# Kernel tuning notes

Hardware: AMD Instinct MI355X
Metric: run time of the kernel (lower is better)

The kernel has to match this reference:

```python
import jax, jax.numpy as jnp
import numpy as np

N_HEADS = 2
EPS = 1e-5
NEG_SLOPE = 0.02
N_CENTROIDS = 1024
RADII = (0.1, 0.2)
KS = (32, 64)


def fps(x, m):
    # Farthest point sampling (deterministic start at index 0). x: [B, C, N]
    B, C, N = x.shape
    def body(carry, _):
        distance, farthest = carry
        centroid = jnp.take_along_axis(x, jnp.broadcast_to(farthest[:, None, None], (B, C, 1)), axis=2)
        dist = jnp.sum((x - centroid) ** 2, axis=1)  # [B, N]
        distance = jnp.minimum(distance, dist)
        nxt = jnp.argmax(distance, axis=1).astype(jnp.int32)
        return (distance, nxt), farthest
    init = (jnp.full((B, N), 1e10, x.dtype), jnp.zeros((B,), jnp.int32))
    _, idxs = jax.lax.scan(body, init, None, length=m)
    return idxs.T  # [B, m]


def ball_group(x, centroids, radius, k):
    # x: [B, C, N], centroids: [B, C, M] -> (idx [B,M,k] int32, mask [B,M,k] bool)
    B, C, N = x.shape
    M = centroids.shape[2]
    d = (jnp.sum(x * x, axis=1)[:, None, :]
         - 2.0 * jnp.einsum('bcm,bcn->bmn', centroids, x)
         + jnp.sum(centroids * centroids, axis=1)[:, :, None])  # [B, M, N]
    idx = jnp.broadcast_to(jnp.arange(N, dtype=jnp.int32)[None, None, :], (B, M, N))
    idx = jnp.where(d > radius * radius, N, idx)
    idx = -jax.lax.top_k(-idx, k)[0]  # k smallest indices, ascending (matches torch.topk largest=False)
    mask = idx == N
    first = jnp.where(idx[:, :, :1] == N, 0, idx[:, :, :1])
    idx = jnp.where(mask, jnp.broadcast_to(first, idx.shape), idx)
    return idx, mask


def attention_mix(x, y, mask, wq, wk, wv, wo):
    # x: [B, C, K] centroids, y: [B, C, K, Np] groups, mask: [B, K, Np]
    B, C, K = x.shape
    Np = y.shape[3]
    H = N_HEADS
    q = jnp.einsum('oc,bck->bok', wq, x).reshape(B, H, C, K)
    kk = jnp.einsum('oc,bckn->bokn', wk, y).reshape(B, H, C, K, Np)
    v = jnp.einsum('oc,bckn->bokn', wv, y).reshape(B, H, C, K, Np)
    w = jnp.einsum('bhck,bhckn->bhkn', q, kk) / (C ** 0.5)
    w = jnp.where(mask[:, None, :, :], -1e9, w)
    w = jax.nn.softmax(w, axis=3)
    o = jnp.einsum('bhkn,bhckn->bhck', w, v).reshape(B, H * C, K)
    return jnp.einsum('oc,bck->bok', wo, o) + x


def conv_bn(x, w, b, g, beta, act):
    # 1x1 Conv1d + BatchNorm1d (training-mode batch stats) + optional LeakyReLU(0.02)
    x = jnp.einsum('oc,bck->bok', w, x) + b[None, :, None]
    mu = jnp.mean(x, axis=(0, 2), keepdims=True)
    var = jnp.var(x, axis=(0, 2), keepdims=True)
    x = (x - mu) * jax.lax.rsqrt(var + EPS) * g[None, :, None] + beta[None, :, None]
    return jnp.where(x > 0, x, NEG_SLOPE * x) if act else x


def pointnet_msg(xyz, point_features, attn_params, mlp_params):
    support = jnp.concatenate([xyz, point_features], axis=1)  # [B, 32, N]
    B, Cs, N = support.shape
    M = N_CENTROIDS
    cidx = fps(support, M)  # [B, M]
    centroids = jnp.take_along_axis(support, jnp.broadcast_to(cidx[:, None, :], (B, Cs, M)), axis=2)
    new_xyz = jnp.take_along_axis(xyz, jnp.broadcast_to(cidx[:, None, :], (B, 3, M)), axis=2)
    feats = []
    for s, (radius, k) in enumerate(zip(RADII, KS)):
        idx, mask = ball_group(support, centroids, radius, k)  # [B, M, k]
        gidx = jnp.broadcast_to(idx.reshape(B, 1, M * k), (B, Cs, M * k))
        group = jnp.take_along_axis(support, gidx, axis=2).reshape(B, Cs, M, k)
        group = group - centroids[:, :, :, None]
        f = attention_mix(centroids, group, mask, *attn_params[s])
        (w0, b0, g0, t0), (w1, b1, g1, t1) = mlp_params[s]
        f = conv_bn(f, w0, b0, g0, t0, act=True)
        f = conv_bn(f, w1, b1, g1, t1, act=False)
        feats.append(f)
    return new_xyz, jnp.concatenate(feats, axis=1)  # [B,3,M], [B,256,M]


def setup_inputs() -> dict:
    key = jax.random.key(0)
    ks = jax.random.split(key, 32)
    B, N, C = 4, 16384, 32
    d = {}
    d['xyz'] = jax.random.uniform(ks[0], (B, 3, N), jnp.float32)
    d['point_features'] = jax.random.normal(ks[1], (B, C - 3, N), jnp.float32)
    i = 2
    for s in range(2):
        d[f'aq{s}'] = 0.05 * jax.random.normal(ks[i], (64, 32), jnp.float32); i += 1
        d[f'ak{s}'] = 0.05 * jax.random.normal(ks[i], (64, 32), jnp.float32); i += 1
        d[f'av{s}'] = 0.05 * jax.random.normal(ks[i], (64, 32), jnp.float32); i += 1
        d[f'ao{s}'] = 0.05 * jax.random.normal(ks[i], (32, 64), jnp.float32); i += 1
        d[f'mw{s}0'] = 0.05 * jax.random.normal(ks[i], (64, 32), jnp.float32); i += 1
        d[f'mb{s}0'] = jnp.zeros((64,), jnp.float32)
        d[f'mg{s}0'] = jnp.ones((64,), jnp.float32)
        d[f'mbt{s}0'] = jnp.zeros((64,), jnp.float32)
        d[f'mw{s}1'] = 0.05 * jax.random.normal(ks[i], (128, 64), jnp.float32); i += 1
        d[f'mb{s}1'] = jnp.zeros((128,), jnp.float32)
        d[f'mg{s}1'] = jnp.ones((128,), jnp.float32)
        d[f'mbt{s}1'] = jnp.zeros((128,), jnp.float32)
    return d


def reference(xyz, point_features,
              aq0, ak0, av0, ao0, mw00, mb00, mg00, mbt00, mw01, mb01, mg01, mbt01,
              aq1, ak1, av1, ao1, mw10, mb10, mg10, mbt10, mw11, mb11, mg11, mbt11):
    attn_params = (((aq0, ak0, av0, ao0)), ((aq1, ak1, av1, ao1)))
    mlp_params = (((mw00, mb00, mg00, mbt00), (mw01, mb01, mg01, mbt01)),
                  ((mw10, mb10, mg10, mbt10), (mw11, mb11, mg11, mbt11)))
    return pointnet_msg(xyz, point_features, attn_params, mlp_params)
```

## Files before the change

kernel.cpp:

```cpp
#include <hip/hip_runtime.h>
#include <hip/hip_bf16.h>


static constexpr int Bb = 4;
static constexpr int Npts = 16384;
static constexpr int Mc = 1024;
static constexpr int NBLK = 16;
static constexpr int OUT_EXPECT = 12288 + 1048576;
#define BN_EPS 1e-5f
#define SLOPE 0.02f
#define SCOPE_AGT __HIP_MEMORY_SCOPE_AGENT

static constexpr size_t OFF_STATS = 33024;
static constexpr size_t OFF_GCNT  = 40960;
static constexpr size_t ZERO_BYTES = 65536;
static constexpr size_t OFF_CIDX  = 65536;
static constexpr size_t OFF_IDX0  = 81920;
static constexpr size_t OFF_CNT0  = 344064;
static constexpr size_t OFF_IDX1  = 360448;
static constexpr size_t OFF_CNT1  = 884736;
static constexpr size_t OFF_ATTN  = 901120;
static constexpr size_t OFF_Z0    = 1163264;
static constexpr size_t WS_REQUIRED = 1687552;
static constexpr size_t OFF_FSLOT = 901120;
static constexpr size_t FSLOT_BYTES = (size_t)Bb * Mc * NBLK * 8;
static constexpr size_t OFF_Z1 = 1687552;
static constexpr size_t OFF_GENT = OFF_Z1;
static constexpr size_t WS_Z1_REQUIRED = OFF_Z1 + (size_t)Bb * 128 * Mc * 4;
static constexpr size_t OFF_SUPT = WS_Z1_REQUIRED;
static constexpr size_t WS_T_REQUIRED = OFF_SUPT + (size_t)Bb * Npts * 32 * 4;

__device__ __forceinline__ float sup_at(const float* xyz, const float* pf,
                                        int b, int c, int n) {
  return (c < 3) ? xyz[((size_t)b*3 + c)*Npts + n]
                 : pf[((size_t)b*29 + (c-3))*Npts + n];
}

__device__ __forceinline__ float sanf(float v, float repl) {
  if (!(v == v) || fabsf(v) > 1e30f) v = repl;
  return v;
}

__global__ __launch_bounds__(256) void fill_kernel(float* out, int n, float val) {
  int i = blockIdx.x * 256 + threadIdx.x;
  if (i < n) out[i] = val;
}

__global__ __launch_bounds__(256) void buildT_kernel(
    const float* __restrict__ xyz, const float* __restrict__ pf,
    float* __restrict__ supT) {
  int idx = blockIdx.x * 256 + threadIdx.x;
  int n = idx & (Npts - 1);
  int b = idx >> 14;
  float* dst = supT + ((size_t)b * Npts + n) * 32;
#pragma unroll
  for (int c = 0; c < 32; ++c) dst[c] = sup_at(xyz, pf, b, c, n);
}

__global__ __launch_bounds__(512, 2) void fps_ball_kernel(
    const float* __restrict__ xyz, const float* __restrict__ pf,
    const float* __restrict__ supT,
    unsigned int* __restrict__ cidx, unsigned long long* __restrict__ slots,
    unsigned int* __restrict__ gcnt, unsigned int* __restrict__ gent) {
  const int tid = threadIdx.x;
  if (blockIdx.x < 64) {
    const int blk = blockIdx.x;
    const int b = blk >> 4;
    const int sb = blk & (NBLK - 1);
    const int lane = tid & 63, wid = tid >> 6;
    float f0[32], f1[32];
    const int p0 = sb * 1024 + tid;
    const int p1 = p0 + 512;
    float d0 = 1e10f, d1 = 1e10f;
#pragma unroll
    for (int c = 0; c < 32; ++c) {
      f0[c] = sup_at(xyz, pf, b, c, p0);
      f1[c] = sup_at(xyz, pf, b, c, p1);
    }
    __shared__ float cf[32];
    __shared__ unsigned long long red[8];
    if (sb == 0 && tid == 0) atomicExch(&cidx[b * Mc], 0u);
    if (tid < 32) cf[tid] = sup_at(xyz, pf, b, tid, 0);
    __syncthreads();
    unsigned long long* slotb = slots + (size_t)b * Mc * NBLK;
    const float* supTb = supT + (size_t)b * Npts * 32;
    for (int it = 0; it < Mc - 1; ++it) {
      float cc[32];
#pragma unroll
      for (int c = 0; c < 32; ++c) cc[c] = cf[c];
      {
        float d = 0.f, e = 0.f;
#pragma unroll
        for (int c = 0; c < 32; ++c) {
          float t0 = f0[c] - cc[c];
          float s0 = __fmul_rn(t0, t0);
          d = (c == 0) ? s0 : __fadd_rn(d, s0);
          float t1 = f1[c] - cc[c];
          float s1 = __fmul_rn(t1, t1);
          e = (c == 0) ? s1 : __fadd_rn(e, s1);
        }
        d0 = fminf(d0, d);
        d1 = fminf(d1, e);
      }
      float bd; int bp;
      if (d0 >= d1) { bd = d0; bp = p0; } else { bd = d1; bp = p1; }
      unsigned long long v =
          ((unsigned long long)__float_as_uint(bd) << 32) | (unsigned int)(~(unsigned int)bp);
#pragma unroll
      for (int d = 32; d; d >>= 1) {
        unsigned long long o = __shfl_xor(v, d, 64);
        if (o > v) v = o;
      }
      if (lane == 0) red[wid] = v;
      __syncthreads();
      if (tid == 0) {
        unsigned long long vb = red[0];
#pragma unroll
        for (int w = 1; w < 8; ++w) if (red[w] > vb) vb = red[w];
        atomicMax(&slotb[(size_t)it * NBLK + sb], vb);
      }
      if (wid == 0) {
        unsigned long long myv = 0;
        if (lane < NBLK) {
          const unsigned long long* sp = &slotb[(size_t)it * NBLK + lane];
          while ((myv = __hip_atomic_load(sp, __ATOMIC_RELAXED, SCOPE_AGT)) == 0ull)
            __builtin_amdgcn_s_sleep(1);
        }
        unsigned long long mv = myv;
#pragma unroll
        for (int d = 8; d; d >>= 1) {
          unsigned long long o = __shfl_xor(mv, d, 16);
          if (o > mv) mv = o;
        }
        unsigned long long vwin = __shfl(mv, 0, 64);
        int idxWin = (int)(~(unsigned int)(vwin & 0xffffffffu)) & (Npts - 1);
        if (lane < 32) cf[lane] = supTb[(size_t)idxWin * 32 + lane];
        if (lane == 0 && sb == 0)
          atomicExch(&cidx[b * Mc + it + 1], (unsigned int)idxWin);
      }
      __syncthreads();
    }
  } else {
    const int blk2 = blockIdx.x - 64;
    const int b = blk2 >> 5;
    const int chunk = blk2 & 31;
    const int p = chunk * 512 + tid;
    const float* supTb = supT + (size_t)b * Npts * 32;
    float x[32];
    const float* srow = supTb + (size_t)p * 32;
#pragma unroll
    for (int c = 0; c < 32; ++c) x[c] = srow[c];
    float sp = 0.f;
#pragma unroll
    for (int c = 0; c < 32; ++c) sp = fmaf(x[c], x[c], sp);
    __shared__ float cfb[2][32];
    unsigned int* cidxb = cidx + b * Mc;
    unsigned int* gcntb = gcnt + b * Mc;
    unsigned int* gentb = gent + (size_t)b * Mc * 128;
    for (int m = 0; m < Mc; ++m) {
      if (tid < 32) {
        unsigned int ci;
        const unsigned int* cp = &cidxb[m];
        while ((ci = __hip_atomic_load(cp, __ATOMIC_RELAXED, SCOPE_AGT)) == 0xFFFFFFFFu)
          __builtin_amdgcn_s_sleep(2);
        cfb[m & 1][tid] = supTb[(size_t)(ci & (Npts - 1)) * 32 + tid];
      }
      __syncthreads();
      const float* cfm = cfb[m & 1];
      float csq = 0.f, dot = 0.f;
#pragma unroll
      for (int c = 0; c < 32; ++c) {
        csq = fmaf(cfm[c], cfm[c], csq);
        dot = fmaf(cfm[c], x[c], dot);
      }
      float d = sp - 2.0f * dot + csq;
      if (d <= 0.04f) {
        int pos = atomicAdd(&gcntb[m], 1u);
        if (pos < 128)
          gentb[(size_t)m * 128 + pos] = (unsigned int)p | (d <= 0.01f ? 0x80000000u : 0u);
      }
    }
  }
}

__global__ __launch_bounds__(256) void ballpost_kernel(
    unsigned int* __restrict__ gcnt, unsigned int* __restrict__ gent,
    unsigned short* __restrict__ idx0, int* __restrict__ cnt0,
    unsigned short* __restrict__ idx1, int* __restrict__ cnt1) {
  int idx = blockIdx.x * 256 + threadIdx.x;
  int b = idx >> 10;
  int m = idx & (Mc - 1);
  int gm = b * Mc + m;
  unsigned int* e = gent + (size_t)gm * 128;
  int nn = (int)gcnt[gm]; if (nn > 128) nn = 128;
  for (int i = 1; i < nn; ++i) {
    unsigned int ei = e[i]; unsigned int key = ei & 0x7fffffffu;
    int j = i - 1;
    while (j >= 0 && (e[j] & 0x7fffffffu) > key) { e[j+1] = e[j]; --j; }
    e[j+1] = ei;
  }
  int c1 = nn < 64 ? nn : 64;
  unsigned short first1 = nn > 0 ? (unsigned short)(e[0] & 0x7fffffffu) : 0;
  unsigned short* o1 = idx1 + (size_t)gm * 64;
  for (int j = 0; j < 64; ++j)
    o1[j] = j < c1 ? (unsigned short)(e[j] & 0x7fffffffu) : first1;
  cnt1[gm] = c1;
  unsigned short* o0 = idx0 + (size_t)gm * 32;
  int c0 = 0; unsigned short first0 = 0;
  for (int i = 0; i < nn && c0 < 32; ++i) {
    if (e[i] & 0x80000000u) {
      unsigned short nv = (unsigned short)(e[i] & 0x7fffffffu);
      if (c0 == 0) first0 = nv;
      o0[c0++] = nv;
    }
  }
  for (int j = c0; j < 32; ++j) o0[j] = first0;
  cnt0[gm] = c0;
}

__global__ __launch_bounds__(512, 2) void fps_kernel(
    const float* __restrict__ xyz, const float* __restrict__ pf,
    const float* __restrict__ supT,
    int* __restrict__ cidx, unsigned long long* __restrict__ slots) {
  const int blk = blockIdx.x;
  const int b = blk >> 4;
  const int sb = blk & (NBLK - 1);
  const int tid = threadIdx.x;
  const int lane = tid & 63, wid = tid >> 6;
  float f0[32], f1[32];
  const int p0 = sb * 1024 + tid;
  const int p1 = p0 + 512;
  float d0 = 1e10f, d1 = 1e10f;
#pragma unroll
  for (int c = 0; c < 32; ++c) {
    f0[c] = sup_at(xyz, pf, b, c, p0);
    f1[c] = sup_at(xyz, pf, b, c, p1);
  }
  __shared__ float cf[32];
  __shared__ unsigned long long red[8];
  if (sb == 0 && tid == 0) cidx[b * Mc] = 0;
  if (tid < 32) cf[tid] = sup_at(xyz, pf, b, tid, 0);
  __syncthreads();
  unsigned long long* slotb = slots + (size_t)b * Mc * NBLK;
  const float* supTb = supT ? supT + (size_t)b * Npts * 32 : nullptr;
  for (int it = 0; it < Mc - 1; ++it) {
    float cc[32];
#pragma unroll
    for (int c = 0; c < 32; ++c) cc[c] = cf[c];
    {
      float d = 0.f, e = 0.f;
#pragma unroll
      for (int c = 0; c < 32; ++c) {
        float t0 = f0[c] - cc[c];
        float s0 = __fmul_rn(t0, t0);
        d = (c == 0) ? s0 : __fadd_rn(d, s0);
        float t1 = f1[c] - cc[c];
        float s1 = __fmul_rn(t1, t1);
        e = (c == 0) ? s1 : __fadd_rn(e, s1);
      }
      d0 = fminf(d0, d);
      d1 = fminf(d1, e);
    }
    float bd; int bp;
    if (d0 >= d1) { bd = d0; bp = p0; } else { bd = d1; bp = p1; }
    unsigned long long v =
        ((unsigned long long)__float_as_uint(bd) << 32) | (unsigned int)(~(unsigned int)bp);
#pragma unroll
    for (int d = 32; d; d >>= 1) {
      unsigned long long o = __shfl_xor(v, d, 64);
      if (o > v) v = o;
    }
    if (lane == 0) red[wid] = v;
    __syncthreads();
    if (tid == 0) {
      unsigned long long vb = red[0];
#pragma unroll
      for (int w = 1; w < 8; ++w) if (red[w] > vb) vb = red[w];
      atomicMax(&slotb[(size_t)it * NBLK + sb], vb);
    }
    if (wid == 0) {
      unsigned long long myv = 0;
      if (lane < NBLK) {
        const unsigned long long* sp = &slotb[(size_t)it * NBLK + lane];
        while ((myv = __hip_atomic_load(sp, __ATOMIC_RELAXED, SCOPE_AGT)) == 0ull)
          __builtin_amdgcn_s_sleep(1);
      }
      unsigned long long mv = myv;
#pragma unroll
      for (int d = 8; d; d >>= 1) {
        unsigned long long o = __shfl_xor(mv, d, 16);
        if (o > mv) mv = o;
      }
      unsigned long long vwin = __shfl(mv, 0, 64);
      int idxWin = (int)(~(unsigned int)(vwin & 0xffffffffu)) & (Npts - 1);
      if (lane < 32)
        cf[lane] = supTb ? supTb[(size_t)idxWin * 32 + lane]
                         : sup_at(xyz, pf, b, lane, idxWin);
      if (lane == 0 && sb == 0) cidx[b * Mc + it + 1] = idxWin;
    }
    __syncthreads();
  }
}

__global__ __launch_bounds__(256) void gather_kernel(
    const float* __restrict__ xyz, const int* __restrict__ cidx,
    float* __restrict__ oxyz, int out_size) {
  int idx = blockIdx.x * 256 + threadIdx.x;
  if (idx >= out_size || idx >= 12288) return;
  int m = idx & (Mc - 1);
  int t = idx >> 10;
  int b = t / 3;
  int ci = cidx[b * Mc + m] & (Npts - 1);
  oxyz[idx] = sanf(xyz[(size_t)t * Npts + ci], 888.0f);
}

__global__ __launch_bounds__(256) void ball_kernel(
    const float* __restrict__ xyz, const float* __restrict__ pf,
    const int* __restrict__ cidx,
    unsigned short* __restrict__ idx0, int* __restrict__ cnt0,
    unsigned short* __restrict__ idx1, int* __restrict__ cnt1) {
  const int b = blockIdx.x >> 6;
  const int mt = blockIdx.x & 63;
  const int tid = threadIdx.x;
  __shared__ float cf[16][32];
  __shared__ float csq[16];
  __shared__ unsigned int ent[16][128];
  __shared__ int lcnt[16];
  for (int i = tid; i < 16 * 32; i += 256) {
    int ml = i >> 5, c = i & 31;
    int ci = cidx[b * Mc + mt * 16 + ml] & (Npts - 1);
    cf[ml][c] = sup_at(xyz, pf, b, c, ci);
  }
  if (tid < 16) lcnt[tid] = 0;
  __syncthreads();
  if (tid < 16) {
    float a = 0.f;
#pragma unroll
    for (int c = 0; c < 32; ++c) a = fmaf(cf[tid][c], cf[tid][c], a);
    csq[tid] = a;
  }
  __syncthreads();
  for (int ch = 0; ch < Npts / 256; ++ch) {
    int p = ch * 256 + tid;
    float x[32];
#pragma unroll
    for (int c = 0; c < 32; ++c) x[c] = sup_at(xyz, pf, b, c, p);
    float sp = 0.f;
#pragma unroll
    for (int c = 0; c < 32; ++c) sp = fmaf(x[c], x[c], sp);
#pragma unroll 4
    for (int ml = 0; ml < 16; ++ml) {
      float dot = 0.f;
#pragma unroll
      for (int c = 0; c < 32; ++c) dot = fmaf(cf[ml][c], x[c], dot);
      float d = sp - 2.0f * dot + csq[ml];
      if (d <= 0.04f) {
        int pos = atomicAdd(&lcnt[ml], 1);
        if (pos < 128) ent[ml][pos] = (unsigned int)p | (d <= 0.01f ? 0x80000000u : 0u);
      }
    }
  }
  __syncthreads();
  if (tid < 16) {
    int ml = tid;
    int nn = lcnt[ml]; if (nn > 128) nn = 128;
    for (int i = 1; i < nn; ++i) {
      unsigned int e = ent[ml][i]; unsigned int key = e & 0x7fffffffu;
      int j = i - 1;
      while (j >= 0 && (ent[ml][j] & 0x7fffffffu) > key) { ent[ml][j+1] = ent[ml][j]; --j; }
      ent[ml][j+1] = e;
    }
    int gm = b * Mc + mt * 16 + ml;
    int c1 = nn < 64 ? nn : 64;
    unsigned short first1 = nn > 0 ? (unsigned short)(ent[ml][0] & 0x7fffffffu) : 0;
    unsigned short* o1 = idx1 + (size_t)gm * 64;
    for (int j = 0; j < 64; ++j)
      o1[j] = j < c1 ? (unsigned short)(ent[ml][j] & 0x7fffffffu) : first1;
    cnt1[gm] = c1;
    unsigned short* o0 = idx0 + (size_t)gm * 32;
    int c0 = 0; unsigned short first0 = 0;
    for (int i = 0; i < nn && c0 < 32; ++i) {
      if (ent[ml][i] & 0x80000000u) {
        unsigned short nv = (unsigned short)(ent[ml][i] & 0x7fffffffu);
        if (c0 == 0) first0 = nv;
        o0[c0++] = nv;
      }
    }
    for (int j = c0; j < 32; ++j) o0[j] = first0;
    cnt0[gm] = c0;
  }
}

template <int K>
__global__ __launch_bounds__(256) void attn_kernel(
    const float* __restrict__ xyz, const float* __restrict__ pf,
    const float* __restrict__ supT,
    const int* __restrict__ cidx,
    const unsigned short* __restrict__ idxS, const int* __restrict__ cntS,
    const float* __restrict__ wq, const float* __restrict__ wk,
    const float* __restrict__ wv, const float* __restrict__ wo,
    __hip_bfloat16* __restrict__ outA) {
  __shared__ float WqL[64*33], WkL[64*33], WvL[64*33], WoL[32*65];
  __shared__ float xv[4][32];
  __shared__ float qv[4][64];
  __shared__ float yb[4][2][32];
  __shared__ float ov[4][64];
  __shared__ int cns[4];
  const int tid = threadIdx.x;
  const int wid = tid >> 6, lane = tid & 63;
  const int gid = blockIdx.x;
  const int b = gid >> 8;
  const int m = ((gid & 255) << 2) + wid;
  const float* supTb = supT ? supT + (size_t)b * Npts * 32 : nullptr;
  for (int i = tid; i < 2048; i += 256) {
    int r = i >> 5, c = i & 31;
    WqL[r*33 + c] = wq[i];
    WkL[r*33 + c] = wk[i];
    WvL[r*33 + c] = wv[i];
    int ro = i >> 6, co = i & 63;
    WoL[ro*65 + co] = wo[i];
  }
  if (lane < 32) {
    int ci = cidx[b * Mc + m] & (Npts - 1);
    xv[wid][lane] = supTb ? supTb[(size_t)ci * 32 + lane]
                          : sup_at(xyz, pf, b, lane, ci);
  }
  if (lane == 0) cns[wid] = cntS[b * Mc + m];
  __syncthreads();
  {
    float acc = 0.f;
#pragma unroll
    for (int c = 0; c < 32; ++c) acc = fmaf(WqL[lane*33 + c], xv[wid][c], acc);
    qv[wid][lane] = acc;
  }
  __syncthreads();
  int cnt = cns[wid];
  cnt = cnt < 1 ? 1 : (cnt > K ? K : cnt);
  const int jj = lane < K ? lane : 0;
  int nj = (int)idxS[((size_t)b*Mc + m)*K + jj] & (Npts - 1);
  float y[32];
  if (supTb) {
    const float* yr = supTb + (size_t)nj * 32;
#pragma unroll
    for (int c = 0; c < 32; ++c) y[c] = yr[c] - xv[wid][c];
  } else {
#pragma unroll
    for (int c = 0; c < 32; ++c) y[c] = sup_at(xyz, pf, b, c, nj) - xv[wid][c];
  }
  float w0 = 0.f, w1 = 0.f;
#pragma unroll 2
  for (int r = 0; r < 32; ++r) {
    float k0 = 0.f, k1 = 0.f;
#pragma unroll
    for (int c = 0; c < 32; ++c) {
      k0 = fmaf(WkL[r*33 + c], y[c], k0);
      k1 = fmaf(WkL[(r+32)*33 + c], y[c], k1);
    }
    w0 = fmaf(qv[wid][r], k0, w0);
    w1 = fmaf(qv[wid][r+32], k1, w1);
  }
  const float iscale = 0.17677669529663689f;
  w0 *= iscale; w1 *= iscale;
  if (lane >= cnt) { w0 = -1e9f; w1 = -1e9f; }
  float mx0 = w0, mx1 = w1;
#pragma unroll
  for (int d = K/2; d; d >>= 1) {
    mx0 = fmaxf(mx0, __shfl_xor(mx0, d, K));
    mx1 = fmaxf(mx1, __shfl_xor(mx1, d, K));
  }
  float e0 = __expf(w0 - mx0), e1 = __expf(w1 - mx1);
  float s0 = e0, s1 = e1;
#pragma unroll
  for (int d = K/2; d; d >>= 1) {
    s0 += __shfl_xor(s0, d, K);
    s1 += __shfl_xor(s1, d, K);
  }
  float wn0 = e0 / s0, wn1 = e1 / s1;
#pragma unroll
  for (int c = 0; c < 32; ++c) {
    float t0 = wn0 * y[c], t1 = wn1 * y[c];
#pragma unroll
    for (int d = K/2; d; d >>= 1) {
      t0 += __shfl_xor(t0, d, K);
      t1 += __shfl_xor(t1, d, K);
    }
    if (lane == 0) { yb[wid][0][c] = t0; yb[wid][1][c] = t1; }
  }
  __syncthreads();
  {
    const int h = lane >> 5;
    float a2 = 0.f;
#pragma unroll
    for (int c = 0; c < 32; ++c) a2 = fmaf(WvL[lane*33 + c], yb[wid][h][c], a2);
    ov[wid][lane] = a2;
  }
  __syncthreads();
  if (lane < 32) {
    float a3 = 0.f;
#pragma unroll
    for (int r = 0; r < 64; ++r) a3 = fmaf(WoL[lane*65 + r], ov[wid][r], a3);
    outA[((size_t)b*32 + lane)*Mc + m] = __float2bfloat16(a3 + xv[wid][lane]);
  }
}

__global__ __launch_bounds__(256) void conv0_kernel(
    const __hip_bfloat16* __restrict__ inA, const float* __restrict__ w0,
    const float* __restrict__ b0, __hip_bfloat16* __restrict__ z0,
    float* __restrict__ ssum, float* __restrict__ ssq) {
  int idx = blockIdx.x * 256 + threadIdx.x;
  int m = idx & (Mc - 1);
  int r = (idx >> 10) & 63;
  int b = idx >> 16;
  float acc = b0[r];
#pragma unroll
  for (int c = 0; c < 32; ++c)
    acc = fmaf(w0[r*32 + c], __bfloat162float(inA[((size_t)b*32 + c)*Mc + m]), acc);
  z0[((size_t)b*64 + r)*Mc + m] = __float2bfloat16(acc);
  float s = acc, q = acc * acc;
#pragma unroll
  for (int d = 32; d; d >>= 1) { s += __shfl_down(s, d, 64); q += __shfl_down(q, d, 64); }
  if ((threadIdx.x & 63) == 0) { atomicAdd(&ssum[r], s); atomicAdd(&ssq[r], q); }
}

__global__ __launch_bounds__(256) void conv1_stats_kernel(
    const __hip_bfloat16* __restrict__ z0,
    const float* __restrict__ ssum0, const float* __restrict__ ssq0,
    const float* __restrict__ g0, const float* __restrict__ t0,
    const float* __restrict__ w1, const float* __restrict__ b1,
    float* __restrict__ z1,
    float* __restrict__ ssum1, float* __restrict__ ssq1) {
  __shared__ float A0s[64], B0s[64];
  int tid = threadIdx.x;
  if (tid < 64) {
    float mu = ssum0[tid] * (1.0f/4096.0f);
    float var = ssq0[tid] * (1.0f/4096.0f) - mu * mu;
    if (var < 0.f) var = 0.f;
    float a = g0[tid] * rsqrtf(var + BN_EPS);
    A0s[tid] = a;
    B0s[tid] = t0[tid] - mu * a;
  }
  __syncthreads();
  int idx = blockIdx.x * 256 + tid;
  int m = idx & (Mc - 1);
  int r2 = (idx >> 10) & 127;
  int b = idx >> 17;
  float acc = b1[r2];
#pragma unroll 8
  for (int r = 0; r < 64; ++r) {
    float u = fmaf(__bfloat162float(z0[((size_t)b*64 + r)*Mc + m]), A0s[r], B0s[r]);
    u = u > 0.f ? u : SLOPE * u;
    acc = fmaf(w1[r2*64 + r], u, acc);
  }
  if (z1) z1[idx] = acc;
  float s = acc, q = acc * acc;
#pragma unroll
  for (int d = 32; d; d >>= 1) { s += __shfl_down(s, d, 64); q += __shfl_down(q, d, 64); }
  if ((tid & 63) == 0) { atomicAdd(&ssum1[r2], s); atomicAdd(&ssq1[r2], q); }
}

__global__ __launch_bounds__(256) void conv1_write_kernel(
    const __hip_bfloat16* __restrict__ z0, const float* __restrict__ z1,
    const float* __restrict__ ssum0, const float* __restrict__ ssq0,
    const float* __restrict__ g0, const float* __restrict__ t0,
    const float* __restrict__ w1, const float* __restrict__ b1,
    const float* __restrict__ ssum1, const float* __restrict__ ssq1,
    const float* __restrict__ g1, const float* __restrict__ t1,
    float* __restrict__ outAll, int chOff, int out_size) {
  __shared__ float A0s[64], B0s[64];
  __shared__ float ab1[2];
  int tid = threadIdx.x;
  int idx = blockIdx.x * 256 + tid;
  int m = idx & (Mc - 1);
  int r2 = (idx >> 10) & 127;
  int b = idx >> 17;
  if (!z1 && tid < 64) {
    float mu = ssum0[tid] * (1.0f/4096.0f);
    float var = ssq0[tid] * (1.0f/4096.0f) - mu * mu;
    if (var < 0.f) var = 0.f;
    float a = g0[tid] * rsqrtf(var + BN_EPS);
    A0s[tid] = a;
    B0s[tid] = t0[tid] - mu * a;
  }
  if (tid == 0) {
    float mu = ssum1[r2] * (1.0f/4096.0f);
    float var = ssq1[r2] * (1.0f/4096.0f) - mu * mu;
    if (var < 0.f) var = 0.f;
    float a = g1[r2] * rsqrtf(var + BN_EPS);
    ab1[0] = a;
    ab1[1] = t1[r2] - mu * a;
  }
  __syncthreads();
  float acc;
  if (z1) {
    acc = z1[idx];
  } else {
    acc = b1[r2];
#pragma unroll 8
    for (int r = 0; r < 64; ++r) {
      float u = fmaf(__bfloat162float(z0[((size_t)b*64 + r)*Mc + m]), A0s[r], B0s[r]);
      u = u > 0.f ? u : SLOPE * u;
      acc = fmaf(w1[r2*64 + r], u, acc);
    }
  }
  float v = fmaf(acc, ab1[0], ab1[1]);
  size_t oidx = 12288 + ((size_t)b*256 + chOff + r2)*Mc + m;
  if (oidx < (size_t)out_size) outAll[oidx] = sanf(v, 777.0f);
}

extern "C" void kernel_launch(void* const* d_in, const int* in_sizes, int n_in,
                              void* d_out, int out_size, void* d_ws, size_t ws_size,
                              hipStream_t stream) {
  float* outb = (float*)d_out;
  int fillBlocks = (out_size + 255) / 256;
  if (n_in != 26 || in_sizes[0] != Bb*3*Npts || in_sizes[1] != Bb*29*Npts
      || in_sizes[2] != 2048) {
    fill_kernel<<<fillBlocks, 256, 0, stream>>>(outb, out_size, 7777.0f);
    return;
  }
  if (out_size != OUT_EXPECT) {
    fill_kernel<<<fillBlocks, 256, 0, stream>>>(outb, out_size, 23456.0f);
    return;
  }
  if (ws_size < WS_REQUIRED) {
    fill_kernel<<<fillBlocks, 256, 0, stream>>>(outb, out_size, 12345.0f);
    return;
  }
  const float* xyz = (const float*)d_in[0];
  const float* pf  = (const float*)d_in[1];
  char* ws = (char*)d_ws;
  int* cidx = (int*)(ws + OFF_CIDX);
  unsigned short* idx0 = (unsigned short*)(ws + OFF_IDX0);
  int* cnt0 = (int*)(ws + OFF_CNT0);
  unsigned short* idx1 = (unsigned short*)(ws + OFF_IDX1);
  int* cnt1 = (int*)(ws + OFF_CNT1);
  unsigned long long* fslots = (unsigned long long*)(ws + OFF_FSLOT);
  __hip_bfloat16* attn = (__hip_bfloat16*)(ws + OFF_ATTN);
  __hip_bfloat16* z0 = (__hip_bfloat16*)(ws + OFF_Z0);
  const bool fused = (ws_size >= WS_T_REQUIRED);
  float* z1 = (ws_size >= WS_Z1_REQUIRED) ? (float*)(ws + OFF_Z1) : nullptr;
  float* supT = fused ? (float*)(ws + OFF_SUPT) : nullptr;
  unsigned int* gcnt = (unsigned int*)(ws + OFF_GCNT);
  unsigned int* gent = (unsigned int*)(ws + OFF_GENT);

  hipMemsetAsync(ws, 0, ZERO_BYTES, stream);
  hipMemsetAsync(ws + OFF_FSLOT, 0, FSLOT_BYTES, stream);
  if (fused) {
    hipMemsetAsync(ws + OFF_CIDX, 0xFF, Bb * Mc * 4, stream);
    buildT_kernel<<<Bb*Npts/256, 256, 0, stream>>>(xyz, pf, supT);
    fps_ball_kernel<<<192, 512, 0, stream>>>(xyz, pf, supT, (unsigned int*)cidx,
                                             fslots, gcnt, gent);
    ballpost_kernel<<<16, 256, 0, stream>>>(gcnt, gent, idx0, cnt0, idx1, cnt1);
  } else {
    fps_kernel<<<Bb*NBLK, 512, 0, stream>>>(xyz, pf, supT, cidx, fslots);
    ball_kernel<<<Bb*64, 256, 0, stream>>>(xyz, pf, cidx, idx0, cnt0, idx1, cnt1);
  }

  for (int s = 0; s < 2; ++s) {
    const float* aq = (const float*)d_in[2 + s*12 + 0];
    const float* ak = (const float*)d_in[2 + s*12 + 1];
    const float* av = (const float*)d_in[2 + s*12 + 2];
    const float* ao = (const float*)d_in[2 + s*12 + 3];
    const float* w0 = (const float*)d_in[2 + s*12 + 4];
    const float* b0 = (const float*)d_in[2 + s*12 + 5];
    const float* g0 = (const float*)d_in[2 + s*12 + 6];
    const float* t0 = (const float*)d_in[2 + s*12 + 7];
    const float* w1 = (const float*)d_in[2 + s*12 + 8];
    const float* b1 = (const float*)d_in[2 + s*12 + 9];
    const float* g1 = (const float*)d_in[2 + s*12 + 10];
    const float* t1 = (const float*)d_in[2 + s*12 + 11];
    float* st = (float*)(ws + OFF_STATS) + (size_t)s*384;
    float *sum0 = st, *sq0 = st + 64, *sum1 = st + 128, *sq1 = st + 256;
    if (s == 0)
      attn_kernel<32><<<Bb*Mc/4, 256, 0, stream>>>(xyz, pf, supT, cidx, idx0, cnt0,
                                                   aq, ak, av, ao, attn);
    else
      attn_kernel<64><<<Bb*Mc/4, 256, 0, stream>>>(xyz, pf, supT, cidx, idx1, cnt1,
                                                   aq, ak, av, ao, attn);
    conv0_kernel<<<Bb*64*Mc/256, 256, 0, stream>>>(attn, w0, b0, z0, sum0, sq0);
    conv1_stats_kernel<<<Bb*128*Mc/256, 256, 0, stream>>>(z0, sum0, sq0, g0, t0,
                                                          w1, b1, z1, sum1, sq1);
    conv1_write_kernel<<<Bb*128*Mc/256, 256, 0, stream>>>(z0, z1, sum0, sq0, g0, t0,
                                                          w1, b1, sum1, sq1, g1, t1,
                                                          outb, s*128, out_size);
  }
  gather_kernel<<<48, 256, 0, stream>>>(xyz, cidx, outb, out_size);
}
```

Baseline: 2.689 ms.

## Batch both scales' attention and conv stages into combined kernel launches

Runs the attention, conv0, conv1-stats and conv1-write stages for both radii scales in a single launch each, using separate workspace buffers for the second scale. This halves the number of launches in the post-grouping pipeline and doubles the grid per launch, aiming to cut launch overhead and improve GPU fill. It also raises the sleep interval in the spin-wait on centroid indices inside the fused FPS/ball kernel. The combined path needs a larger workspace and falls back to the old per-scale loop when the workspace is too small.

```diff
diff --git a/kernel.cpp b/kernel.cpp
--- a/kernel.cpp
+++ b/kernel.cpp
@@ -29,6 +29,10 @@
 static constexpr size_t WS_Z1_REQUIRED = OFF_Z1 + (size_t)Bb * 128 * Mc * 4;
 static constexpr size_t OFF_SUPT = WS_Z1_REQUIRED;
 static constexpr size_t WS_T_REQUIRED = OFF_SUPT + (size_t)Bb * Npts * 32 * 4;
+static constexpr size_t OFF_ATTN1 = WS_T_REQUIRED;
+static constexpr size_t OFF_Z01   = OFF_ATTN1 + (size_t)Bb * 32 * Mc * 2;
+static constexpr size_t OFF_Z11   = OFF_Z01 + (size_t)Bb * 64 * Mc * 2;
+static constexpr size_t WS_EXT_REQUIRED = OFF_Z11 + (size_t)Bb * 128 * Mc * 4;
 
 __device__ __forceinline__ float sup_at(const float* xyz, const float* pf,
                                         int b, int c, int n) {
@@ -162,7 +166,7 @@
         unsigned int ci;
         const unsigned int* cp = &cidxb[m];
         while ((ci = __hip_atomic_load(cp, __ATOMIC_RELAXED, SCOPE_AGT)) == 0xFFFFFFFFu)
-          __builtin_amdgcn_s_sleep(2);
+          __builtin_amdgcn_s_sleep(16);
         cfb[m & 1][tid] = supTb[(size_t)(ci & (Npts - 1)) * 32 + tid];
       }
       __syncthreads();
@@ -392,10 +396,108 @@
 }
 
 template <int K>
+__device__ __forceinline__ void attn_body(
+    const float* xyz, const float* pf, const float* supTb,
+    const int* cidx, const unsigned short* idxS, const int* cntS,
+    const float* wq, const float* wk, const float* wv, const float* wo,
+    __hip_bfloat16* outA, int b, int m, int wid, int lane, int tid,
+    float* WqL, float* WkL, float* WvL, float* WoL,
+    float (*xv)[32], float (*qv)[64], float (*yb)[2][32], float (*ov)[64], int* cns) {
+  for (int i = tid; i < 2048; i += 256) {
+    int r = i >> 5, c = i & 31;
+    WqL[r*33 + c] = wq[i];
+    WkL[r*33 + c] = wk[i];
+    WvL[r*33 + c] = wv[i];
+    int ro = i >> 6, co = i & 63;
+    WoL[ro*65 + co] = wo[i];
+  }
+  if (lane < 32) {
+    int ci = cidx[b * Mc + m] & (Npts - 1);
+    xv[wid][lane] = supTb ? supTb[(size_t)ci * 32 + lane]
+                          : sup_at(xyz, pf, b, lane, ci);
+  }
+  if (lane == 0) cns[wid] = cntS[b * Mc + m];
+  __syncthreads();
+  {
+    float acc = 0.f;
+#pragma unroll
+    for (int c = 0; c < 32; ++c) acc = fmaf(WqL[lane*33 + c], xv[wid][c], acc);
+    qv[wid][lane] = acc;
+  }
+  __syncthreads();
+  int cnt = cns[wid];
+  cnt = cnt < 1 ? 1 : (cnt > K ? K : cnt);
+  const int jj = lane < K ? lane : 0;
+  int nj = (int)idxS[((size_t)b*Mc + m)*K + jj] & (Npts - 1);
+  float y[32];
+  if (supTb) {
+    const float* yr = supTb + (size_t)nj * 32;
+#pragma unroll
+    for (int c = 0; c < 32; ++c) y[c] = yr[c] - xv[wid][c];
+  } else {
+#pragma unroll
+    for (int c = 0; c < 32; ++c) y[c] = sup_at(xyz, pf, b, c, nj) - xv[wid][c];
+  }
+  float w0 = 0.f, w1 = 0.f;
+#pragma unroll 2
+  for (int r = 0; r < 32; ++r) {
+    float k0 = 0.f, k1 = 0.f;
+#pragma unroll
+    for (int c = 0; c < 32; ++c) {
+      k0 = fmaf(WkL[r*33 + c], y[c], k0);
+      k1 = fmaf(WkL[(r+32)*33 + c], y[c], k1);
+    }
+    w0 = fmaf(qv[wid][r], k0, w0);
+    w1 = fmaf(qv[wid][r+32], k1, w1);
+  }
+  const float iscale = 0.17677669529663689f;
+  w0 *= iscale; w1 *= iscale;
+  if (lane >= cnt) { w0 = -1e9f; w1 = -1e9f; }
+  float mx0 = w0, mx1 = w1;
+#pragma unroll
+  for (int d = K/2; d; d >>= 1) {
+    mx0 = fmaxf(mx0, __shfl_xor(mx0, d, K));
+    mx1 = fmaxf(mx1, __shfl_xor(mx1, d, K));
+  }
+  float e0 = __expf(w0 - mx0), e1 = __expf(w1 - mx1);
+  float s0 = e0, s1 = e1;
+#pragma unroll
+  for (int d = K/2; d; d >>= 1) {
+    s0 += __shfl_xor(s0, d, K);
+    s1 += __shfl_xor(s1, d, K);
+  }
+  float wn0 = e0 / s0, wn1 = e1 / s1;
+#pragma unroll
+  for (int c = 0; c < 32; ++c) {
+    float t0 = wn0 * y[c], t1 = wn1 * y[c];
+#pragma unroll
+    for (int d = K/2; d; d >>= 1) {
+      t0 += __shfl_xor(t0, d, K);
+      t1 += __shfl_xor(t1, d, K);
+    }
+    if (lane == 0) { yb[wid][0][c] = t0; yb[wid][1][c] = t1; }
+  }
+  __syncthreads();
+  {
+    const int h = lane >> 5;
+    float a2 = 0.f;
+#pragma unroll
+    for (int c = 0; c < 32; ++c) a2 = fmaf(WvL[lane*33 + c], yb[wid][h][c], a2);
+    ov[wid][lane] = a2;
+  }
+  __syncthreads();
+  if (lane < 32) {
+    float a3 = 0.f;
+#pragma unroll
+    for (int r = 0; r < 64; ++r) a3 = fmaf(WoL[lane*65 + r], ov[wid][r], a3);
+    outA[((size_t)b*32 + lane)*Mc + m] = __float2bfloat16(a3 + xv[wid][lane]);
+  }
+}
+
+template <int K>
 __global__ __launch_bounds__(256) void attn_kernel(
     const float* __restrict__ xyz, const float* __restrict__ pf,
-    const float* __restrict__ supT,
-    const int* __restrict__ cidx,
+    const float* __restrict__ supT, const int* __restrict__ cidx,
     const unsigned short* __restrict__ idxS, const int* __restrict__ cntS,
     const float* __restrict__ wq, const float* __restrict__ wk,
     const float* __restrict__ wv, const float* __restrict__ wo,
@@ -412,125 +514,83 @@
   const int b = gid >> 8;
   const int m = ((gid & 255) << 2) + wid;
   const float* supTb = supT ? supT + (size_t)b * Npts * 32 : nullptr;
-  for (int i = tid; i < 2048; i += 256) {
-    int r = i >> 5, c = i & 31;
-    WqL[r*33 + c] = wq[i];
-    WkL[r*33 + c] = wk[i];
-    WvL[r*33 + c] = wv[i];
-    int ro = i >> 6, co = i & 63;
-    WoL[ro*65 + co] = wo[i];
-  }
-  if (lane < 32) {
-    int ci = cidx[b * Mc + m] & (Npts - 1);
-    xv[wid][lane] = supTb ? supTb[(size_t)ci * 32 + lane]
-                          : sup_at(xyz, pf, b, lane, ci);
-  }
-  if (lane == 0) cns[wid] = cntS[b * Mc + m];
-  __syncthreads();
-  {
-    float acc = 0.f;
-#pragma unroll
-    for (int c = 0; c < 32; ++c) acc = fmaf(WqL[lane*33 + c], xv[wid][c], acc);
-    qv[wid][lane] = acc;
-  }
-  __syncthreads();
-  int cnt = cns[wid];
-  cnt = cnt < 1 ? 1 : (cnt > K ? K : cnt);
-  const int jj = lane < K ? lane : 0;
-  int nj = (int)idxS[((size_t)b*Mc + m)*K + jj] & (Npts - 1);
-  float y[32];
-  if (supTb) {
-    const float* yr = supTb + (size_t)nj * 32;
-#pragma unroll
-    for (int c = 0; c < 32; ++c) y[c] = yr[c] - xv[wid][c];
-  } else {
-#pragma unroll
-    for (int c = 0; c < 32; ++c) y[c] = sup_at(xyz, pf, b, c, nj) - xv[wid][c];
-  }
-  float w0 = 0.f, w1 = 0.f;
-#pragma unroll 2
-  for (int r = 0; r < 32; ++r) {
-    float k0 = 0.f, k1 = 0.f;
-#pragma unroll
-    for (int c = 0; c < 32; ++c) {
-      k0 = fmaf(WkL[r*33 + c], y[c], k0);
-      k1 = fmaf(WkL[(r+32)*33 + c], y[c], k1);
-    }
-    w0 = fmaf(qv[wid][r], k0, w0);
-    w1 = fmaf(qv[wid][r+32], k1, w1);
-  }
-  const float iscale = 0.17677669529663689f;
-  w0 *= iscale; w1 *= iscale;
-  if (lane >= cnt) { w0 = -1e9f; w1 = -1e9f; }
-  float mx0 = w0, mx1 = w1;
-#pragma unroll
-  for (int d = K/2; d; d >>= 1) {
-    mx0 = fmaxf(mx0, __shfl_xor(mx0, d, K));
-    mx1 = fmaxf(mx1, __shfl_xor(mx1, d, K));
-  }
-  float e0 = __expf(w0 - mx0), e1 = __expf(w1 - mx1);
-  float s0 = e0, s1 = e1;
-#pragma unroll
-  for (int d = K/2; d; d >>= 1) {
-    s0 += __shfl_xor(s0, d, K);
-    s1 += __shfl_xor(s1, d, K);
-  }
-  float wn0 = e0 / s0, wn1 = e1 / s1;
-#pragma unroll
-  for (int c = 0; c < 32; ++c) {
-    float t0 = wn0 * y[c], t1 = wn1 * y[c];
-#pragma unroll
-    for (int d = K/2; d; d >>= 1) {
-      t0 += __shfl_xor(t0, d, K);
-      t1 += __shfl_xor(t1, d, K);
-    }
-    if (lane == 0) { yb[wid][0][c] = t0; yb[wid][1][c] = t1; }
-  }
-  __syncthreads();
-  {
-    const int h = lane >> 5;
-    float a2 = 0.f;
-#pragma unroll
-    for (int c = 0; c < 32; ++c) a2 = fmaf(WvL[lane*33 + c], yb[wid][h][c], a2);
-    ov[wid][lane] = a2;
-  }
-  __syncthreads();
-  if (lane < 32) {
-    float a3 = 0.f;
-#pragma unroll
-    for (int r = 0; r < 64; ++r) a3 = fmaf(WoL[lane*65 + r], ov[wid][r], a3);
-    outA[((size_t)b*32 + lane)*Mc + m] = __float2bfloat16(a3 + xv[wid][lane]);
-  }
+  attn_body<K>(xyz, pf, supTb, cidx, idxS, cntS, wq, wk, wv, wo, outA,
+               b, m, wid, lane, tid, WqL, WkL, WvL, WoL, xv, qv, yb, ov, cns);
+}
+
+__global__ __launch_bounds__(256) void attn_comb_kernel(
+    const float* __restrict__ xyz, const float* __restrict__ pf,
+    const float* __restrict__ supT, const int* __restrict__ cidx,
+    const unsigned short* __restrict__ idx0, const int* __restrict__ cnt0,
+    const unsigned short* __restrict__ idx1, const int* __restrict__ cnt1,
+    const float* __restrict__ wq0, const float* __restrict__ wk0,
+    const float* __restrict__ wv0, const float* __restrict__ wo0,
+    const float* __restrict__ wq1, const float* __restrict__ wk1,
+    const float* __restrict__ wv1, const float* __restrict__ wo1,
+    __hip_bfloat16* __restrict__ attn0, __hip_bfloat16* __restrict__ attn1) {
+  __shared__ float WqL[64*33], WkL[64*33], WvL[64*33], WoL[32*65];
+  __shared__ float xv[4][32];
+  __shared__ float qv[4][64];
+  __shared__ float yb[4][2][32];
+  __shared__ float ov[4][64];
+  __shared__ int cns[4];
+  const int tid = threadIdx.x;
+  const int wid = tid >> 6, lane = tid & 63;
+  const int s = blockIdx.x >> 10;
+  const int gid = blockIdx.x & 1023;
+  const int b = gid >> 8;
+  const int m = ((gid & 255) << 2) + wid;
+  const float* supTb = supT + (size_t)b * Npts * 32;
+  if (s == 0)
+    attn_body<32>(xyz, pf, supTb, cidx, idx0, cnt0, wq0, wk0, wv0, wo0, attn0,
+                  b, m, wid, lane, tid, WqL, WkL, WvL, WoL, xv, qv, yb, ov, cns);
+  else
+    attn_body<64>(xyz, pf, supTb, cidx, idx1, cnt1, wq1, wk1, wv1, wo1, attn1,
+                  b, m, wid, lane, tid, WqL, WkL, WvL, WoL, xv, qv, yb, ov, cns);
+}
+
+__device__ __forceinline__ void conv0_body(
+    const __hip_bfloat16* inA, const float* w0, const float* b0,
+    __hip_bfloat16* z0, float* ssum, float* ssq, int idx, int tid) {
+  int m = idx & (Mc - 1);
+  int r = (idx >> 10) & 63;
+  int b = idx >> 16;
+  float acc = b0[r];
+#pragma unroll
+  for (int c = 0; c < 32; ++c)
+    acc = fmaf(w0[r*32 + c], __bfloat162float(inA[((size_t)b*32 + c)*Mc + m]), acc);
+  z0[((size_t)b*64 + r)*Mc + m] = __float2bfloat16(acc);
+  float s = acc, q = acc * acc;
+#pragma unroll
+  for (int d = 32; d; d >>= 1) { s += __shfl_down(s, d, 64); q += __shfl_down(q, d, 64); }
+  if ((tid & 63) == 0) { atomicAdd(&ssum[r], s); atomicAdd(&ssq[r], q); }
 }
 
 __global__ __launch_bounds__(256) void conv0_kernel(
     const __hip_bfloat16* __restrict__ inA, const float* __restrict__ w0,
     const float* __restrict__ b0, __hip_bfloat16* __restrict__ z0,
     float* __restrict__ ssum, float* __restrict__ ssq) {
-  int idx = blockIdx.x * 256 + threadIdx.x;
-  int m = idx & (Mc - 1);
-  int r = (idx >> 10) & 63;
-  int b = idx >> 16;
-  float acc = b0[r];
-#pragma unroll
-  for (int c = 0; c < 32; ++c)
-    acc = fmaf(w0[r*32 + c], __bfloat162float(inA[((size_t)b*32 + c)*Mc + m]), acc);
-  z0[((size_t)b*64 + r)*Mc + m] = __float2bfloat16(acc);
-  float s = acc, q = acc * acc;
-#pragma unroll
-  for (int d = 32; d; d >>= 1) { s += __shfl_down(s, d, 64); q += __shfl_down(q, d, 64); }
-  if ((threadIdx.x & 63) == 0) { atomicAdd(&ssum[r], s); atomicAdd(&ssq[r], q); }
-}
-
-__global__ __launch_bounds__(256) void conv1_stats_kernel(
-    const __hip_bfloat16* __restrict__ z0,
-    const float* __restrict__ ssum0, const float* __restrict__ ssq0,
-    const float* __restrict__ g0, const float* __restrict__ t0,
-    const float* __restrict__ w1, const float* __restrict__ b1,
-    float* __restrict__ z1,
-    float* __restrict__ ssum1, float* __restrict__ ssq1) {
+  conv0_body(inA, w0, b0, z0, ssum, ssq, blockIdx.x * 256 + threadIdx.x, threadIdx.x);
+}
+
+__global__ __launch_bounds__(256) void conv0_comb_kernel(
+    const __hip_bfloat16* __restrict__ attn0, const __hip_bfloat16* __restrict__ attn1,
+    const float* __restrict__ w00, const float* __restrict__ b00,
+    const float* __restrict__ w01, const float* __restrict__ b01,
+    __hip_bfloat16* __restrict__ z00, __hip_bfloat16* __restrict__ z01,
+    float* __restrict__ st) {
+  int s = blockIdx.x >> 10;
+  int idx = (blockIdx.x & 1023) * 256 + threadIdx.x;
+  float* stS = st + (size_t)s * 384;
+  if (s == 0) conv0_body(attn0, w00, b00, z00, stS, stS + 64, idx, threadIdx.x);
+  else        conv0_body(attn1, w01, b01, z01, stS, stS + 64, idx, threadIdx.x);
+}
+
+__device__ __forceinline__ void conv1_stats_body(
+    const __hip_bfloat16* z0, const float* ssum0, const float* ssq0,
+    const float* g0, const float* t0, const float* w1, const float* b1,
+    float* z1, float* ssum1, float* ssq1, int idx, int tid) {
   __shared__ float A0s[64], B0s[64];
-  int tid = threadIdx.x;
   if (tid < 64) {
     float mu = ssum0[tid] * (1.0f/4096.0f);
     float var = ssq0[tid] * (1.0f/4096.0f) - mu * mu;
@@ -540,7 +600,6 @@
     B0s[tid] = t0[tid] - mu * a;
   }
   __syncthreads();
-  int idx = blockIdx.x * 256 + tid;
   int m = idx & (Mc - 1);
   int r2 = (idx >> 10) & 127;
   int b = idx >> 17;
@@ -556,6 +615,56 @@
 #pragma unroll
   for (int d = 32; d; d >>= 1) { s += __shfl_down(s, d, 64); q += __shfl_down(q, d, 64); }
   if ((tid & 63) == 0) { atomicAdd(&ssum1[r2], s); atomicAdd(&ssq1[r2], q); }
+}
+
+__global__ __launch_bounds__(256) void conv1_stats_kernel(
+    const __hip_bfloat16* __restrict__ z0,
+    const float* __restrict__ ssum0, const float* __restrict__ ssq0,
+    const float* __restrict__ g0, const float* __restrict__ t0,
+    const float* __restrict__ w1, const float* __restrict__ b1,
+    float* __restrict__ z1, float* __restrict__ ssum1, float* __restrict__ ssq1) {
+  conv1_stats_body(z0, ssum0, ssq0, g0, t0, w1, b1, z1, ssum1, ssq1,
+                   blockIdx.x * 256 + threadIdx.x, threadIdx.x);
+}
+
+__global__ __launch_bounds__(256) void conv1_stats_comb_kernel(
+    const __hip_bfloat16* __restrict__ z00, const __hip_bfloat16* __restrict__ z01,
+    const float* __restrict__ g00, const float* __restrict__ t00,
+    const float* __restrict__ w10, const float* __restrict__ b10,
+    const float* __restrict__ g01, const float* __restrict__ t01,
+    const float* __restrict__ w11, const float* __restrict__ b11,
+    float* __restrict__ z10, float* __restrict__ z11, float* __restrict__ st) {
+  int s = blockIdx.x >> 11;
+  int idx = (blockIdx.x & 2047) * 256 + threadIdx.x;
+  float* stS = st + (size_t)s * 384;
+  if (s == 0)
+    conv1_stats_body(z00, stS, stS + 64, g00, t00, w10, b10, z10, stS + 128, stS + 256,
+                     idx, threadIdx.x);
+  else
+    conv1_stats_body(z01, stS, stS + 64, g01, t01, w11, b11, z11, stS + 128, stS + 256,
+                     idx, threadIdx.x);
+}
+
+__device__ __forceinline__ void conv1_write_body(
+    const float* z1, const float* ssum1, const float* ssq1,
+    const float* g1, const float* t1, float* outAll, int chOff, int out_size,
+    int idx, int tid) {
+  __shared__ float ab1[2];
+  int m = idx & (Mc - 1);
+  int r2 = (idx >> 10) & 127;
+  int b = idx >> 17;
+  if (tid == 0) {
+    float mu = ssum1[r2] * (1.0f/4096.0f);
+    float var = ssq1[r2] * (1.0f/4096.0f) - mu * mu;
+    if (var < 0.f) var = 0.f;
+    float a = g1[r2] * rsqrtf(var + BN_EPS);
+    ab1[0] = a;
+    ab1[1] = t1[r2] - mu * a;
+  }
+  __syncthreads();
+  float v = fmaf(z1[idx], ab1[0], ab1[1]);
+  size_t oidx = 12288 + ((size_t)b*256 + chOff + r2)*Mc + m;
+  if (oidx < (size_t)out_size) outAll[oidx] = sanf(v, 777.0f);
 }
 
 __global__ __launch_bounds__(256) void conv1_write_kernel(
@@ -607,6 +716,22 @@
   if (oidx < (size_t)out_size) outAll[oidx] = sanf(v, 777.0f);
 }
 
+__global__ __launch_bounds__(256) void conv1_write_comb_kernel(
+    const float* __restrict__ z10, const float* __restrict__ z11,
+    const float* __restrict__ g10, const float* __restrict__ t10,
+    const float* __restrict__ g11, const float* __restrict__ t11,
+    const float* __restrict__ st, float* __restrict__ outAll, int out_size) {
+  int s = blockIdx.x >> 11;
+  int idx = (blockIdx.x & 2047) * 256 + threadIdx.x;
+  const float* stS = st + (size_t)s * 384;
+  if (s == 0)
+    conv1_write_body(z10, stS + 128, stS + 256, g10, t10, outAll, 0, out_size,
+                     idx, threadIdx.x);
+  else
+    conv1_write_body(z11, stS + 128, stS + 256, g11, t11, outAll, 128, out_size,
+                     idx, threadIdx.x);
+}
+
 extern "C" void kernel_launch(void* const* d_in, const int* in_sizes, int n_in,
                               void* d_out, int out_size, void* d_ws, size_t ws_size,
                               hipStream_t stream) {
@@ -634,13 +759,21 @@
   unsigned short* idx1 = (unsigned short*)(ws + OFF_IDX1);
   int* cnt1 = (int*)(ws + OFF_CNT1);
   unsigned long long* fslots = (unsigned long long*)(ws + OFF_FSLOT);
-  __hip_bfloat16* attn = (__hip_bfloat16*)(ws + OFF_ATTN);
-  __hip_bfloat16* z0 = (__hip_bfloat16*)(ws + OFF_Z0);
+  __hip_bfloat16* attn0 = (__hip_bfloat16*)(ws + OFF_ATTN);
+  __hip_bfloat16* z00 = (__hip_bfloat16*)(ws + OFF_Z0);
   const bool fused = (ws_size >= WS_T_REQUIRED);
-  float* z1 = (ws_size >= WS_Z1_REQUIRED) ? (float*)(ws + OFF_Z1) : nullptr;
+  const bool comb = (ws_size >= WS_EXT_REQUIRED);
+  float* z10 = (ws_size >= WS_Z1_REQUIRED) ? (float*)(ws + OFF_Z1) : nullptr;
   float* supT = fused ? (float*)(ws + OFF_SUPT) : nullptr;
   unsigned int* gcnt = (unsigned int*)(ws + OFF_GCNT);
   unsigned int* gent = (unsigned int*)(ws + OFF_GENT);
+  __hip_bfloat16* attn1 = comb ? (__hip_bfloat16*)(ws + OFF_ATTN1) : nullptr;
+  __hip_bfloat16* z01 = comb ? (__hip_bfloat16*)(ws + OFF_Z01) : nullptr;
+  float* z11 = comb ? (float*)(ws + OFF_Z11) : nullptr;
+  float* st = (float*)(ws + OFF_STATS);
+
+  const float *W[24];
+  for (int i = 0; i < 24; ++i) W[i] = (const float*)d_in[2 + i];
 
   hipMemsetAsync(ws, 0, ZERO_BYTES, stream);
   hipMemsetAsync(ws + OFF_FSLOT, 0, FSLOT_BYTES, stream);
@@ -655,33 +788,36 @@
     ball_kernel<<<Bb*64, 256, 0, stream>>>(xyz, pf, cidx, idx0, cnt0, idx1, cnt1);
   }
 
-  for (int s = 0; s < 2; ++s) {
-    const float* aq = (const float*)d_in[2 + s*12 + 0];
-    const float* ak = (const float*)d_in[2 + s*12 + 1];
-    const float* av = (const float*)d_in[2 + s*12 + 2];
-    const float* ao = (const float*)d_in[2 + s*12 + 3];
-    const float* w0 = (const float*)d_in[2 + s*12 + 4];
-    const float* b0 = (const float*)d_in[2 + s*12 + 5];
-    const float* g0 = (const float*)d_in[2 + s*12 + 6];
-    const float* t0 = (const float*)d_in[2 + s*12 + 7];
-    const float* w1 = (const float*)d_in[2 + s*12 + 8];
-    const float* b1 = (const float*)d_in[2 + s*12 + 9];
-    const float* g1 = (const float*)d_in[2 + s*12 + 10];
-    const float* t1 = (const float*)d_in[2 + s*12 + 11];
-    float* st = (float*)(ws + OFF_STATS) + (size_t)s*384;
-    float *sum0 = st, *sq0 = st + 64, *sum1 = st + 128, *sq1 = st + 256;
-    if (s == 0)
-      attn_kernel<32><<<Bb*Mc/4, 256, 0, stream>>>(xyz, pf, supT, cidx, idx0, cnt0,
-                                                   aq, ak, av, ao, attn);
-    else
-      attn_kernel<64><<<Bb*Mc/4, 256, 0, stream>>>(xyz, pf, supT, cidx, idx1, cnt1,
-                                                   aq, ak, av, ao, attn);
-    conv0_kernel<<<Bb*64*Mc/256, 256, 0, stream>>>(attn, w0, b0, z0, sum0, sq0);
-    conv1_stats_kernel<<<Bb*128*Mc/256, 256, 0, stream>>>(z0, sum0, sq0, g0, t0,
-                                                          w1, b1, z1, sum1, sq1);
-    conv1_write_kernel<<<Bb*128*Mc/256, 256, 0, stream>>>(z0, z1, sum0, sq0, g0, t0,
-                                                          w1, b1, sum1, sq1, g1, t1,
-                                                          outb, s*128, out_size);
+  if (comb) {
+    attn_comb_kernel<<<2048, 256, 0, stream>>>(xyz, pf, supT, cidx,
+        idx0, cnt0, idx1, cnt1,
+        W[0], W[1], W[2], W[3], W[12], W[13], W[14], W[15], attn0, attn1);
+    conv0_comb_kernel<<<2048, 256, 0, stream>>>(attn0, attn1,
+        W[4], W[5], W[16], W[17], z00, z01, st);
+    conv1_stats_comb_kernel<<<4096, 256, 0, stream>>>(z00, z01,
+        W[6], W[7], W[8], W[9], W[18], W[19], W[20], W[21], z10, z11, st);
+    conv1_write_comb_kernel<<<4096, 256, 0, stream>>>(z10, z11,
+        W[10], W[11], W[22], W[23], st, outb, out_size);
+  } else {
+    for (int s = 0; s < 2; ++s) {
+      const float *aq = W[s*12+0], *ak = W[s*12+1], *av = W[s*12+2], *ao = W[s*12+3];
+      const float *w0 = W[s*12+4], *b0 = W[s*12+5], *g0 = W[s*12+6], *t0 = W[s*12+7];
+      const float *w1 = W[s*12+8], *b1 = W[s*12+9], *g1 = W[s*12+10], *t1 = W[s*12+11];
+      float* stS = st + (size_t)s*384;
+      float *sum0 = stS, *sq0 = stS + 64, *sum1 = stS + 128, *sq1 = stS + 256;
+      if (s == 0)
+        attn_kernel<32><<<Bb*Mc/4, 256, 0, stream>>>(xyz, pf, supT, cidx, idx0, cnt0,
+                                                     aq, ak, av, ao, attn0);
+      else
+        attn_kernel<64><<<Bb*Mc/4, 256, 0, stream>>>(xyz, pf, supT, cidx, idx1, cnt1,
+                                                     aq, ak, av, ao, attn0);
+      conv0_kernel<<<Bb*64*Mc/256, 256, 0, stream>>>(attn0, w0, b0, z00, sum0, sq0);
+      conv1_stats_kernel<<<Bb*128*Mc/256, 256, 0, stream>>>(z00, sum0, sq0, g0, t0,
+                                                            w1, b1, z10, sum1, sq1);
+      conv1_write_kernel<<<Bb*128*Mc/256, 256, 0, stream>>>(z00, z10, sum0, sq0, g0, t0,
+                                                            w1, b1, sum1, sq1, g1, t1,
+                                                            outb, s*128, out_size);
+    }
   }
   gather_kernel<<<48, 256, 0, stream>>>(xyz, cidx, outb, out_size);
 }
```

Result: faster. 2.608 ms (-3.0%).
